# Performance work log

Hardware: AMD Instinct MI355X
Metric: run time of the kernel (lower is better)

Reference implementation:

```python
import jax, jax.numpy as jnp
import numpy as np

TOPK = 2


def setup_inputs() -> dict:
    key = jax.random.key(0)
    k0, k1, k2, k3, k4 = jax.random.split(key, 5)
    B, S, D, E, H = 4, 2048, 1024, 8, 2816
    return {
        "x": jax.random.normal(k0, (B, S, D), dtype=jnp.float32),
        "gate_w": jax.random.normal(k1, (E, D), dtype=jnp.float32) * 0.02,
        "w1": jax.random.normal(k2, (E, H, D), dtype=jnp.float32) * 0.02,
        "w2": jax.random.normal(k3, (E, D, H), dtype=jnp.float32) * 0.02,
        "w3": jax.random.normal(k4, (E, H, D), dtype=jnp.float32) * 0.02,
    }


def reference(x, gate_w, w1, w2, w3):
    B, S, D = x.shape
    E = gate_w.shape[0]
    T = B * S
    xf = x.reshape(T, D)

    # Router: top-k logits, softmax over the selected k, scatter into a
    # dense [T, E] combine-weight matrix (equivalent to the index_add combine).
    logits = xf @ gate_w.T                      # [T, E]
    tw, ti = jax.lax.top_k(logits, TOPK)        # [T, k]
    tw = jax.nn.softmax(tw, axis=-1)
    cw = jnp.zeros((T, E), dtype=xf.dtype).at[
        jnp.arange(T)[:, None], ti
    ].add(tw)                                   # [T, E] combine weights

    # Expert SwiGLU FFNs, combined with routing weights. Loop over the small
    # fixed expert count; tokens with cw==0 contribute zero, matching the
    # masked dispatch in the original module.
    out = jnp.zeros_like(xf)
    for e in range(E):
        h = jax.nn.silu(xf @ w1[e].T) * (xf @ w3[e].T)   # [T, H]
        out = out + cw[:, e:e + 1] * (h @ w2[e].T)       # [T, D]
    return out.reshape(B, S, D)
```

## Files before the change

kernel.cpp:

```cpp
#include <hip/hip_runtime.h>
#include <stdint.h>

#define T_TOK 8192
#define DIM   1024
#define NEXP  8
#define HID   2816

typedef __bf16 bf16x8 __attribute__((ext_vector_type(8)));
typedef float  f32x4  __attribute__((ext_vector_type(4)));

typedef __attribute__((address_space(3))) uint32_t lds_u32_t;
typedef __attribute__((address_space(1))) const uint32_t gbl_u32_t;

__device__ __forceinline__ void gl_lds16(const void* g, void* l) {
    __builtin_amdgcn_global_load_lds((gbl_u32_t*)g, (lds_u32_t*)l, 16, 0, 0);
}

__device__ __forceinline__ uint32_t f2bf_u(float f) {
    uint32_t u = __builtin_bit_cast(uint32_t, f);
    return u + 0x7fffu + ((u >> 16) & 1u);
}
__device__ __forceinline__ uint32_t pack2(float a, float b) {
    return (f2bf_u(a) >> 16) | (f2bf_u(b) & 0xffff0000u);
}


__global__ __launch_bounds__(256) void cvt_k(
    const float* __restrict__ s, unsigned short* __restrict__ d, int n8)
{
    int i = blockIdx.x * 256 + threadIdx.x;
    if (i < n8) {
        const float4* sp = (const float4*)(s + (size_t)i * 8);
        float4 a = sp[0], b = sp[1];
        uint4 o;
        o.x = pack2(a.x, a.y); o.y = pack2(a.z, a.w);
        o.z = pack2(b.x, b.y); o.w = pack2(b.z, b.w);
        ((uint4*)d)[i] = o;
    }
}

__global__ __launch_bounds__(256) void router_k(
    const float* __restrict__ x, const float* __restrict__ gw,
    int* __restrict__ cnt, int* __restrict__ slot_list,
    float* __restrict__ slot_w)
{
    const int wave = threadIdx.x >> 6, lane = threadIdx.x & 63;
    const int t = blockIdx.x * 4 + wave;
    const float4* xp = (const float4*)(x + (size_t)t * DIM + lane * 16);
    float4 xv[4];
#pragma unroll
    for (int i = 0; i < 4; ++i) xv[i] = xp[i];

    double lg[NEXP];
#pragma unroll
    for (int e = 0; e < NEXP; ++e) {
        const float4* gp = (const float4*)(gw + (size_t)e * DIM + lane * 16);
        double s = 0.0;
#pragma unroll
        for (int i = 0; i < 4; ++i) {
            float4 g = gp[i];
            s += (double)xv[i].x * g.x + (double)xv[i].y * g.y +
                 (double)xv[i].z * g.z + (double)xv[i].w * g.w;
        }
#pragma unroll
        for (int m = 32; m >= 1; m >>= 1) s += __shfl_xor(s, m, 64);
        lg[e] = s;
    }

    if (lane == 0) {
        int e0 = 0; double b0 = lg[0];
#pragma unroll
        for (int e = 1; e < NEXP; ++e)
            if (lg[e] > b0) { b0 = lg[e]; e0 = e; }
        int e1 = -1; double b1 = -1.0e300;
#pragma unroll
        for (int e = 0; e < NEXP; ++e)
            if (e != e0 && lg[e] > b1) { b1 = lg[e]; e1 = e; }

        float p0 = (float)(1.0 / (1.0 + exp(b1 - b0)));
        float p1 = 1.0f - p0;

        int pos0 = atomicAdd(&cnt[e0], 1);
        slot_list[e0 * T_TOK + pos0] = 2 * t;
        slot_w[2 * t] = p0;
        int pos1 = atomicAdd(&cnt[e1], 1);
        slot_list[e1 * T_TOK + pos1] = 2 * t + 1;
        slot_w[2 * t + 1] = p1;
    }
}

__global__ __launch_bounds__(256) void ffn1_k(
    const unsigned short* __restrict__ xb, const unsigned short* __restrict__ w1b,
    const unsigned short* __restrict__ w3b, const int* __restrict__ cnt,
    const int* __restrict__ slot_list, unsigned short* __restrict__ h_ws)
{
    __shared__ unsigned short As[2][128 * 32];
    __shared__ unsigned short B1s[2][64 * 32];
    __shared__ unsigned short B2s[2][64 * 32];
    __shared__ int slots_s[128];

    const int e = blockIdx.z;
    const int cntE = cnt[e];
    const int m0 = blockIdx.y * 128;
    if (m0 >= cntE) return;
    const int n0 = blockIdx.x * 64;
    const int tid = threadIdx.x;
    const int wave = tid >> 6, lane = tid & 63;

    if (tid < 128) {
        int idx = m0 + tid;
        slots_s[tid] = (idx < cntE) ? slot_list[e * T_TOK + idx] : -1;
    }
    __syncthreads();

    const int rr = lane >> 2;
    const int qsw = (lane & 3) ^ ((rr >> 1) & 3);
    const unsigned short* gsrc[4];
    unsigned short* ldst[4];
    int bstride;
    if (wave < 2) {
        bstride = 128 * 32;
#pragma unroll
        for (int i = 0; i < 4; ++i) {
            int row = wave * 64 + i * 16 + rr;
            int slot = slots_s[row];
            int tok = (slot >= 0) ? (slot >> 1) : 0;
            gsrc[i] = xb + (size_t)tok * DIM + qsw * 8;
            ldst[i] = &As[0][(wave * 64 + i * 16) * 32];
        }
    } else if (wave == 2) {
        bstride = 64 * 32;
#pragma unroll
        for (int i = 0; i < 4; ++i) {
            int row = i * 16 + rr;
            gsrc[i] = w1b + ((size_t)e * HID + n0 + row) * DIM + qsw * 8;
            ldst[i] = &B1s[0][(i * 16) * 32];
        }
    } else {
        bstride = 64 * 32;
#pragma unroll
        for (int i = 0; i < 4; ++i) {
            int row = i * 16 + rr;
            gsrc[i] = w3b + ((size_t)e * HID + n0 + row) * DIM + qsw * 8;
            ldst[i] = &B2s[0][(i * 16) * 32];
        }
    }

    const int wm = wave >> 1, wn = wave & 1;
    const int lrow = lane & 15, quad = lane >> 4;
    const int ksw = (quad ^ ((lrow >> 1) & 3)) * 8;

    f32x4 acc1[4][2], acc2[4][2];
    const f32x4 zf = {0.f, 0.f, 0.f, 0.f};
#pragma unroll
    for (int mi = 0; mi < 4; ++mi)
#pragma unroll
        for (int ni = 0; ni < 2; ++ni) { acc1[mi][ni] = zf; acc2[mi][ni] = zf; }

    const int NST = DIM / 32;
#pragma unroll
    for (int i = 0; i < 4; ++i) gl_lds16(gsrc[i], ldst[i]);
#pragma unroll
    for (int i = 0; i < 4; ++i) gsrc[i] += 32;
    __syncthreads();

    for (int t = 0; t < NST; ++t) {
        const int cur = t & 1, nxt = cur ^ 1;
        if (t + 1 < NST) {
#pragma unroll
            for (int i = 0; i < 4; ++i)
                gl_lds16(gsrc[i], ldst[i] + nxt * bstride);
#pragma unroll
            for (int i = 0; i < 4; ++i) gsrc[i] += 32;
        }
        const unsigned short* Ab  = &As[cur][0];
        const unsigned short* B1b = &B1s[cur][0];
        const unsigned short* B2b = &B2s[cur][0];

        bf16x8 af[4], b1f[2], b2f[2];
#pragma unroll
        for (int mi = 0; mi < 4; ++mi)
            af[mi] = *(const bf16x8*)&Ab[(wm * 64 + mi * 16 + lrow) * 32 + ksw];
#pragma unroll
        for (int ni = 0; ni < 2; ++ni) {
            b1f[ni] = *(const bf16x8*)&B1b[(wn * 32 + ni * 16 + lrow) * 32 + ksw];
            b2f[ni] = *(const bf16x8*)&B2b[(wn * 32 + ni * 16 + lrow) * 32 + ksw];
        }
        __builtin_amdgcn_s_setprio(1);
#pragma unroll
        for (int mi = 0; mi < 4; ++mi)
#pragma unroll
            for (int ni = 0; ni < 2; ++ni) {
                acc1[mi][ni] = __builtin_amdgcn_mfma_f32_16x16x32_bf16(
                    af[mi], b1f[ni], acc1[mi][ni], 0, 0, 0);
                acc2[mi][ni] = __builtin_amdgcn_mfma_f32_16x16x32_bf16(
                    af[mi], b2f[ni], acc2[mi][ni], 0, 0, 0);
            }
        __builtin_amdgcn_s_setprio(0);

        if (t + 1 < NST) __syncthreads();
    }

#pragma unroll
    for (int mi = 0; mi < 4; ++mi) {
#pragma unroll
        for (int r = 0; r < 4; ++r) {
            int mloc = wm * 64 + mi * 16 + quad * 4 + r;
            int slot = slots_s[mloc];
            if (slot >= 0) {
                unsigned short* hrow =
                    h_ws + (size_t)slot * HID + n0 + wn * 32 + lrow;
#pragma unroll
                for (int ni = 0; ni < 2; ++ni) {
                    float a1 = acc1[mi][ni][r], a3 = acc2[mi][ni][r];
                    float hv = (a1 / (1.f + __expf(-a1))) * a3;
                    hrow[ni * 16] = (unsigned short)(f2bf_u(hv) >> 16);
                }
            }
        }
    }
}

__global__ __launch_bounds__(256) void ffn2_k(
    const unsigned short* __restrict__ h_ws, const unsigned short* __restrict__ w2b,
    const int* __restrict__ cnt, const int* __restrict__ slot_list,
    const float* __restrict__ slot_w, float* __restrict__ out)
{
    __shared__ unsigned short As[2][128 * 32];
    __shared__ unsigned short Bs[2][128 * 32];
    __shared__ int slots_s[128];
    __shared__ float wgt_s[128];

    const int e = blockIdx.z;
    const int cntE = cnt[e];
    const int m0 = blockIdx.y * 128;
    if (m0 >= cntE) return;
    const int n0 = blockIdx.x * 128;
    const int tid = threadIdx.x;
    const int wave = tid >> 6, lane = tid & 63;

    if (tid < 128) {
        int idx = m0 + tid;
        int s = (idx < cntE) ? slot_list[e * T_TOK + idx] : -1;
        slots_s[tid] = s;
        wgt_s[tid] = (s >= 0) ? slot_w[s] : 0.f;
    }
    __syncthreads();

    const int rr = lane >> 2;
    const int qsw = (lane & 3) ^ ((rr >> 1) & 3);
    const unsigned short* gsrc[4];
    unsigned short* ldst[4];
    const int bstride = 128 * 32;
    if (wave < 2) {
#pragma unroll
        for (int i = 0; i < 4; ++i) {
            int row = wave * 64 + i * 16 + rr;
            int slot = slots_s[row];
            int s = (slot >= 0) ? slot : 0;
            gsrc[i] = h_ws + (size_t)s * HID + qsw * 8;
            ldst[i] = &As[0][(wave * 64 + i * 16) * 32];
        }
    } else {
#pragma unroll
        for (int i = 0; i < 4; ++i) {
            int row = (wave - 2) * 64 + i * 16 + rr;
            gsrc[i] = w2b + ((size_t)e * DIM + n0 + row) * HID + qsw * 8;
            ldst[i] = &Bs[0][((wave - 2) * 64 + i * 16) * 32];
        }
    }

    const int wm = wave >> 1, wn = wave & 1;
    const int lrow = lane & 15, quad = lane >> 4;
    const int ksw = (quad ^ ((lrow >> 1) & 3)) * 8;

    f32x4 acc[4][4];
    const f32x4 zf = {0.f, 0.f, 0.f, 0.f};
#pragma unroll
    for (int mi = 0; mi < 4; ++mi)
#pragma unroll
        for (int ni = 0; ni < 4; ++ni) acc[mi][ni] = zf;

    const int NST = HID / 32;
#pragma unroll
    for (int i = 0; i < 4; ++i) gl_lds16(gsrc[i], ldst[i]);
#pragma unroll
    for (int i = 0; i < 4; ++i) gsrc[i] += 32;
    __syncthreads();

    for (int t = 0; t < NST; ++t) {
        const int cur = t & 1, nxt = cur ^ 1;
        if (t + 1 < NST) {
#pragma unroll
            for (int i = 0; i < 4; ++i)
                gl_lds16(gsrc[i], ldst[i] + nxt * bstride);
#pragma unroll
            for (int i = 0; i < 4; ++i) gsrc[i] += 32;
        }
        const unsigned short* Ab = &As[cur][0];
        const unsigned short* Bb = &Bs[cur][0];

        bf16x8 af[4], bf[4];
#pragma unroll
        for (int mi = 0; mi < 4; ++mi)
            af[mi] = *(const bf16x8*)&Ab[(wm * 64 + mi * 16 + lrow) * 32 + ksw];
#pragma unroll
        for (int ni = 0; ni < 4; ++ni)
            bf[ni] = *(const bf16x8*)&Bb[(wn * 64 + ni * 16 + lrow) * 32 + ksw];
        __builtin_amdgcn_s_setprio(1);
#pragma unroll
        for (int mi = 0; mi < 4; ++mi)
#pragma unroll
            for (int ni = 0; ni < 4; ++ni)
                acc[mi][ni] = __builtin_amdgcn_mfma_f32_16x16x32_bf16(
                    af[mi], bf[ni], acc[mi][ni], 0, 0, 0);
        __builtin_amdgcn_s_setprio(0);

        if (t + 1 < NST) __syncthreads();
    }

#pragma unroll
    for (int mi = 0; mi < 4; ++mi) {
#pragma unroll
        for (int r = 0; r < 4; ++r) {
            int mloc = wm * 64 + mi * 16 + quad * 4 + r;
            int slot = slots_s[mloc];
            if (slot >= 0) {
                int tok = slot >> 1;
                float w = wgt_s[mloc];
                float* orow = out + (size_t)tok * DIM + n0 + wn * 64 + lrow;
#pragma unroll
                for (int ni = 0; ni < 4; ++ni)
                    atomicAdd(&orow[ni * 16], acc[mi][ni][r] * w);
            }
        }
    }
}

extern "C" void kernel_launch(void* const* d_in, const int* in_sizes, int n_in,
                              void* d_out, int out_size, void* d_ws, size_t ws_size,
                              hipStream_t stream) {
    const float* x  = (const float*)d_in[0];
    const float* gw = (const float*)d_in[1];
    const float* w1 = (const float*)d_in[2];
    const float* w2 = (const float*)d_in[3];
    const float* w3 = (const float*)d_in[4];
    float* out = (float*)d_out;

    char* ws = (char*)d_ws;
    int*   cnt       = (int*)ws;
    int*   slot_list = (int*)(ws + 256);
    float* slot_w    = (float*)(ws + 256 + NEXP * T_TOK * 4);
    unsigned short* h_ws = (unsigned short*)(ws + 327936);
    unsigned short* x_bf = (unsigned short*)(ws + 92602624);
    unsigned short* w1_bf = (unsigned short*)(ws + 109379840);
    unsigned short* w3_bf = (unsigned short*)(ws + 155517184);
    unsigned short* w2_bf = (unsigned short*)(ws + 201654528);

    hipMemsetAsync(cnt, 0, 256, stream);
    hipMemsetAsync(out, 0, (size_t)T_TOK * DIM * sizeof(float), stream);

    const int nx = T_TOK * DIM / 8;
    const int nw = NEXP * HID * DIM / 8;
    cvt_k<<<(nx + 255) / 256, 256, 0, stream>>>(x, x_bf, nx);
    cvt_k<<<(nw + 255) / 256, 256, 0, stream>>>(w1, w1_bf, nw);
    cvt_k<<<(nw + 255) / 256, 256, 0, stream>>>(w3, w3_bf, nw);
    cvt_k<<<(nw + 255) / 256, 256, 0, stream>>>(w2, w2_bf, nw);

    router_k<<<T_TOK / 4, 256, 0, stream>>>(x, gw, cnt, slot_list, slot_w);
    ffn1_k<<<dim3(HID / 64, T_TOK / 128, NEXP), 256, 0, stream>>>(
        x_bf, w1_bf, w3_bf, cnt, slot_list, h_ws);
    ffn2_k<<<dim3(DIM / 128, T_TOK / 128, NEXP), 256, 0, stream>>>(
        h_ws, w2_bf, cnt, slot_list, slot_w, out);
}
```

Baseline: 941.0 us.

## Triple-buffer LDS tiles in expert GEMMs with partial vmcnt waits

Both expert FFN GEMM kernels go from double to triple buffering of their LDS tiles. Each step prefetches two stages ahead and waits only until the older stage's loads finish (s_waitcnt vmcnt(4)) before a raw barrier, where __syncthreads used to wait for everything. This is meant to hide more global-load latency behind the MFMA work. The cost is about 50% more LDS per block, which can lower occupancy. The hand-written waitcnt counts must also exactly match the number of loads in flight.

```diff
diff --git a/kernel.cpp b/kernel.cpp
--- a/kernel.cpp
+++ b/kernel.cpp
@@ -94,9 +94,9 @@
     const unsigned short* __restrict__ w3b, const int* __restrict__ cnt,
     const int* __restrict__ slot_list, unsigned short* __restrict__ h_ws)
 {
-    __shared__ unsigned short As[2][128 * 32];
-    __shared__ unsigned short B1s[2][64 * 32];
-    __shared__ unsigned short B2s[2][64 * 32];
+    __shared__ unsigned short As[3][128 * 32];
+    __shared__ unsigned short B1s[3][64 * 32];
+    __shared__ unsigned short B2s[3][64 * 32];
     __shared__ int slots_s[128];
 
     const int e = blockIdx.z;
@@ -161,21 +161,25 @@
 #pragma unroll
     for (int i = 0; i < 4; ++i) gl_lds16(gsrc[i], ldst[i]);
 #pragma unroll
-    for (int i = 0; i < 4; ++i) gsrc[i] += 32;
-    __syncthreads();
-
+    for (int i = 0; i < 4; ++i) gl_lds16(gsrc[i] + 32, ldst[i] + bstride);
+#pragma unroll
+    for (int i = 0; i < 4; ++i) gsrc[i] += 64;
+    asm volatile("s_waitcnt vmcnt(4)" ::: "memory");
+    __builtin_amdgcn_s_barrier();
+    __builtin_amdgcn_sched_barrier(0);
+
+    int b0 = 0, b1 = 1, b2 = 2;
     for (int t = 0; t < NST; ++t) {
-        const int cur = t & 1, nxt = cur ^ 1;
-        if (t + 1 < NST) {
+        if (t + 2 < NST) {
 #pragma unroll
             for (int i = 0; i < 4; ++i)
-                gl_lds16(gsrc[i], ldst[i] + nxt * bstride);
+                gl_lds16(gsrc[i], ldst[i] + b2 * bstride);
 #pragma unroll
             for (int i = 0; i < 4; ++i) gsrc[i] += 32;
         }
-        const unsigned short* Ab  = &As[cur][0];
-        const unsigned short* B1b = &B1s[cur][0];
-        const unsigned short* B2b = &B2s[cur][0];
+        const unsigned short* Ab  = &As[0][0]  + b0 * (128 * 32);
+        const unsigned short* B1b = &B1s[0][0] + b0 * (64 * 32);
+        const unsigned short* B2b = &B2s[0][0] + b0 * (64 * 32);
 
         bf16x8 af[4], b1f[2], b2f[2];
 #pragma unroll
@@ -198,7 +202,15 @@
             }
         __builtin_amdgcn_s_setprio(0);
 
-        if (t + 1 < NST) __syncthreads();
+        if (t + 1 < NST) {
+            if (t + 2 < NST)
+                asm volatile("s_waitcnt vmcnt(4)" ::: "memory");
+            else
+                asm volatile("s_waitcnt vmcnt(0)" ::: "memory");
+            __builtin_amdgcn_s_barrier();
+            __builtin_amdgcn_sched_barrier(0);
+        }
+        int tmp = b0; b0 = b1; b1 = b2; b2 = tmp;
     }
 
 #pragma unroll
@@ -226,8 +238,8 @@
     const int* __restrict__ cnt, const int* __restrict__ slot_list,
     const float* __restrict__ slot_w, float* __restrict__ out)
 {
-    __shared__ unsigned short As[2][128 * 32];
-    __shared__ unsigned short Bs[2][128 * 32];
+    __shared__ unsigned short As[3][128 * 32];
+    __shared__ unsigned short Bs[3][128 * 32];
     __shared__ int slots_s[128];
     __shared__ float wgt_s[128];
 
@@ -285,20 +297,24 @@
 #pragma unroll
     for (int i = 0; i < 4; ++i) gl_lds16(gsrc[i], ldst[i]);
 #pragma unroll
-    for (int i = 0; i < 4; ++i) gsrc[i] += 32;
-    __syncthreads();
-
+    for (int i = 0; i < 4; ++i) gl_lds16(gsrc[i] + 32, ldst[i] + bstride);
+#pragma unroll
+    for (int i = 0; i < 4; ++i) gsrc[i] += 64;
+    asm volatile("s_waitcnt vmcnt(4)" ::: "memory");
+    __builtin_amdgcn_s_barrier();
+    __builtin_amdgcn_sched_barrier(0);
+
+    int b0 = 0, b1 = 1, b2 = 2;
     for (int t = 0; t < NST; ++t) {
-        const int cur = t & 1, nxt = cur ^ 1;
-        if (t + 1 < NST) {
+        if (t + 2 < NST) {
 #pragma unroll
             for (int i = 0; i < 4; ++i)
-                gl_lds16(gsrc[i], ldst[i] + nxt * bstride);
+                gl_lds16(gsrc[i], ldst[i] + b2 * bstride);
 #pragma unroll
             for (int i = 0; i < 4; ++i) gsrc[i] += 32;
         }
-        const unsigned short* Ab = &As[cur][0];
-        const unsigned short* Bb = &Bs[cur][0];
+        const unsigned short* Ab = &As[0][0] + b0 * bstride;
+        const unsigned short* Bb = &Bs[0][0] + b0 * bstride;
 
         bf16x8 af[4], bf[4];
 #pragma unroll
@@ -316,7 +332,15 @@
                     af[mi], bf[ni], acc[mi][ni], 0, 0, 0);
         __builtin_amdgcn_s_setprio(0);
 
-        if (t + 1 < NST) __syncthreads();
+        if (t + 1 < NST) {
+            if (t + 2 < NST)
+                asm volatile("s_waitcnt vmcnt(4)" ::: "memory");
+            else
+                asm volatile("s_waitcnt vmcnt(0)" ::: "memory");
+            __builtin_amdgcn_s_barrier();
+            __builtin_amdgcn_sched_barrier(0);
+        }
+        int tmp = b0; b0 = b1; b1 = b2; b2 = tmp;
     }
 
 #pragma unroll
```

New measurement: 909.2 us. -3.4%, faster.
